# Performance work log

Hardware: AMD Instinct MI355X
Metric: run time of the kernel (lower is better)

## Reference

```python
import jax, jax.numpy as jnp
import numpy as np

N = 1_000_000          # total nodes (atoms)
F = 32                 # node feature dim
K = 16                 # kernels per degree
DEG_COUNTS = [200_000, 300_000, 300_000, 200_000]  # focal nodes per degree 1..4
EPS = 1e-8


def _unit(a):
    # L2-normalize along last axis (CosineSimilarity semantics)
    return a / (jnp.linalg.norm(a, axis=-1, keepdims=True) + EPS)


def setup_inputs() -> dict:
    key = jax.random.key(0)
    ks = jax.random.split(key, 16)
    x = jax.random.normal(ks[0], (N, F), dtype=jnp.float32)
    # selected indices: disjoint partition of all nodes by degree (a permutation)
    perm = jax.random.permutation(ks[1], N)
    sels, off = [], 0
    for c in DEG_COUNTS:
        sels.append(perm[off:off + c].astype(jnp.int64))
        off += c
    inp = {"x": x}
    for d in range(1, 5):
        inp[f"selected_index_deg{d}"] = sels[d - 1]
        inp[f"nei_index_deg{d}"] = jax.random.randint(
            ks[1 + d], (d * DEG_COUNTS[d - 1],), 0, N).astype(jnp.int64)
        inp[f"W_focal{d}"] = jax.random.normal(ks[7 + d], (K, F), dtype=jnp.float32)
        inp[f"W_nei{d}"] = jax.random.normal(ks[11 + d], (K, d, F), dtype=jnp.float32)
    return inp


def _degree_score(x, sel, nei, Wf, Wn, deg):
    # gather receptive field for this degree group
    x_focal = _unit(x[sel])                         # (Nd, F)
    x_nei = _unit(x[nei].reshape(-1, deg, F))       # (Nd, deg, F)
    sc_f = _unit(Wf) @ x_focal.T                    # (K, Nd) cosine vs focal kernel
    sc_n = jnp.einsum('kdf,ndf->kn', _unit(Wn), x_nei) / deg  # mean neighbor cosine
    return sc_f + sc_n                              # (K, Nd)


def reference(x,
              W_focal1, W_nei1, W_focal2, W_nei2,
              W_focal3, W_nei3, W_focal4, W_nei4,
              selected_index_deg1, selected_index_deg2,
              selected_index_deg3, selected_index_deg4,
              nei_index_deg1, nei_index_deg2,
              nei_index_deg3, nei_index_deg4):
    sels = [selected_index_deg1, selected_index_deg2,
            selected_index_deg3, selected_index_deg4]
    neis = [nei_index_deg1, nei_index_deg2, nei_index_deg3, nei_index_deg4]
    Wfs = [W_focal1, W_focal2, W_focal3, W_focal4]
    Wns = [W_nei1, W_nei2, W_nei3, W_nei4]

    out = jnp.zeros((4 * K, N), dtype=x.dtype)  # the `zeros` score matrix
    row, col = 0, 0
    for d in range(1, 5):
        sc = _degree_score(x, sels[d - 1], neis[d - 1], Wfs[d - 1], Wns[d - 1], d)
        nd = sels[d - 1].shape[0]
        out = out.at[row:row + K, col:col + nd].set(sc)
        row += K
        col += nd
    # reorder columns back to original node order (get_reorder_index -> sort)
    order = jnp.argsort(jnp.concatenate(sels))
    return out[:, order].T  # (N, 4*K)
```

## Files before the change

kernel.cpp:

```cpp
#include <hip/hip_runtime.h>
#include <math.h>

#define F 32
#define K 16
#define EPSN 1e-8f
#define NPB 512
#define NPB_FB 256


typedef _Float16 half8 __attribute__((ext_vector_type(8)));
typedef float f32x4  __attribute__((ext_vector_type(4)));
typedef int   i32x2  __attribute__((ext_vector_type(2)));
typedef int   i32x4  __attribute__((ext_vector_type(4)));

#define VMWAIT(N) do { asm volatile("s_waitcnt vmcnt(%0)" :: "n"(N) : "memory"); \
                       __builtin_amdgcn_sched_barrier(0); } while (0)

__global__ __launch_bounds__(256)
void norm_x_kernel(const float* __restrict__ x, _Float16* __restrict__ xh,
                   int nrows)
{
    const int t   = blockIdx.x * 256 + threadIdx.x;
    const int row = t >> 2;
    const int p   = t & 3;
    if (row >= nrows) return;
    const float* xr = x + (size_t)row * F + p * 8;
    const float4 a0 = *(const float4*)xr;
    const float4 a1 = *(const float4*)(xr + 4);
    float ss = a0.x*a0.x + a0.y*a0.y + a0.z*a0.z + a0.w*a0.w
             + a1.x*a1.x + a1.y*a1.y + a1.z*a1.z + a1.w*a1.w;
    ss += __shfl_xor(ss, 1);
    ss += __shfl_xor(ss, 2);
    const float sc = 1.f / (sqrtf(ss) + EPSN);
    half8 h;
    h[0] = (_Float16)(a0.x * sc); h[1] = (_Float16)(a0.y * sc);
    h[2] = (_Float16)(a0.z * sc); h[3] = (_Float16)(a0.w * sc);
    h[4] = (_Float16)(a1.x * sc); h[5] = (_Float16)(a1.y * sc);
    h[6] = (_Float16)(a1.z * sc); h[7] = (_Float16)(a1.w * sc);
    *(half8*)(xh + (size_t)row * F + p * 8) = h;
}

__device__ __forceinline__ void gload16(half8& d, const _Float16* xh,
                                        unsigned row, int kq) {
    const unsigned off = row * 64u + (unsigned)kq * 16u;
    asm volatile("global_load_dwordx4 %0, %1, %2"
                 : "=&v"(d) : "v"(off), "s"(xh) : "memory");
}

__device__ __forceinline__ void gstore(float* out, unsigned off, f32x4 v) {
    asm volatile("global_store_dwordx4 %0, %1, %2"
                 :: "v"(off), "v"(v), "s"(out) : "memory");
}

template<int DEG> struct Idx;
template<> struct Idx<1> { int node; int n0;
    __device__ __forceinline__ int nb(int) const { return n0; } };
template<> struct Idx<2> { int node; i32x2 nn;
    __device__ __forceinline__ int nb(int j) const { return nn[j]; } };
template<> struct Idx<3> { int node; i32x2 nn; int n2;
    __device__ __forceinline__ int nb(int j) const { return j < 2 ? nn[j] : n2; } };
template<> struct Idx<4> { int node; i32x4 nn;
    __device__ __forceinline__ int nb(int j) const { return nn[j]; } };

template<int DEG>
__device__ __forceinline__ void load_idx(Idx<DEG>& d, const int* sel,
                                         const int* nei, int ic) {
    const unsigned so = (unsigned)ic << 2;
    asm volatile("global_load_dword %0, %1, %2"
                 : "=&v"(d.node) : "v"(so), "s"(sel) : "memory");
    const unsigned no = (unsigned)(ic * DEG) << 2;
    if constexpr (DEG == 1)
        asm volatile("global_load_dword %0, %1, %2"
                     : "=&v"(d.n0) : "v"(no), "s"(nei) : "memory");
    else if constexpr (DEG == 2)
        asm volatile("global_load_dwordx2 %0, %1, %2"
                     : "=&v"(d.nn) : "v"(no), "s"(nei) : "memory");
    else if constexpr (DEG == 3) {
        asm volatile("global_load_dwordx2 %0, %1, %2"
                     : "=&v"(d.nn) : "v"(no), "s"(nei) : "memory");
        asm volatile("global_load_dword %0, %1, %2 offset:8"
                     : "=&v"(d.n2) : "v"(no), "s"(nei) : "memory");
    } else
        asm volatile("global_load_dwordx4 %0, %1, %2"
                     : "=&v"(d.nn) : "v"(no), "s"(nei) : "memory");
}

__device__ __forceinline__ f32x4 slab2(half8 b, f32x4 acc,
                                       const _Float16* sWh,
                                       const _Float16* sWl,
                                       int lane, int r) {
    const int aoff = r * 512 + lane * 8;
    const half8 ah = *(const half8*)(sWh + aoff);
    const half8 al = *(const half8*)(sWl + aoff);
    acc = __builtin_amdgcn_mfma_f32_16x16x32_f16(ah, b, acc, 0, 0, 0);
    acc = __builtin_amdgcn_mfma_f32_16x16x32_f16(al, b, acc, 0, 0, 0);
    return acc;
}

template<int DEG>
__device__ __forceinline__ void process_deg(const _Float16* __restrict__ xh,
                                            const int*   __restrict__ sel,
                                            const int*   __restrict__ nei,
                                            const float* __restrict__ Wf,
                                            const float* __restrict__ Wn,
                                            float* __restrict__ out,
                                            int nd, int i0,
                                            _Float16* sWh, _Float16* sWl)
{
    constexpr int R  = DEG + 1;
    constexpr int H  = (DEG <= 2) ? 1 : 2;
    constexpr int C0 = H;
    constexpr int C1 = R - H;
    constexpr int NI = (DEG == 3) ? 3 : 2;
    constexpr int KB = C1 + NI;
    constexpr int KD = C0;
    constexpr int NW = K * R;
    constexpr int ITERS = NPB / 64;
    const int tid = threadIdx.x;

    if (tid < NW) {
        const float* src = (tid < K) ? (Wf + tid * F) : (Wn + (tid - K) * F);
        float ss = 0.f;
        #pragma unroll
        for (int f = 0; f < F; ++f) { const float t = src[f]; ss += t * t; }
        const int t = tid - K;
        const int r = (tid < K) ? 0   : (1 + t % DEG);
        const int k = (tid < K) ? tid : (t / DEG);
        const float sc = (1.f / (sqrtf(ss) + EPSN))
                       * ((r == 0) ? 1.f : 1.f / (float)DEG);
        #pragma unroll
        for (int f = 0; f < F; ++f) {
            const float wv = src[f] * sc;
            const _Float16 hi = (_Float16)wv;
            const _Float16 lo = (_Float16)(wv - (float)hi);
            const int off = r * 512 + (k + 16 * (f >> 3)) * 8 + (f & 7);
            sWh[off] = hi; sWl[off] = lo;
        }
    }
    __syncthreads();

    const int lane = tid & 63;
    const int wv   = tid >> 6;
    const int jcol = lane & 15;
    const int kq   = lane >> 4;
    const int i0w  = i0 + wv * 16 + jcol;

    half8 g0[H], g1[R - H];
    const f32x4 zed = {0.f, 0.f, 0.f, 0.f};

    Idx<DEG> ix, iy;
    { const int ic = (i0w < nd) ? i0w : (nd - 1);
      load_idx<DEG>(ix, sel, nei, ic); }
    { const int i1 = i0w + 64; const int ic = (i1 < nd) ? i1 : (nd - 1);
      load_idx<DEG>(iy, sel, nei, ic); }
    VMWAIT(NI);
    #pragma unroll
    for (int r = 0; r < H; ++r)
        gload16(g0[r], xh, (unsigned)((r == 0) ? ix.node : ix.nb(r-1)), kq);

#define ITER(T, XC, YN)                                                        \
    {                                                                          \
        const int nodeT = XC.node;                                             \
        _Pragma("unroll")                                                      \
        for (int r = H; r < R; ++r)                        \
            gload16(g1[r - H], xh, (unsigned)XC.nb(r-1), kq);                  \
        { const int ii = i0w + ((T) + 2) * 64;         \
          load_idx<DEG>(XC, sel, nei, (ii < nd) ? ii : (nd - 1)); }            \
        VMWAIT(KB);                            \
        f32x4 acc = {0.f, 0.f, 0.f, 0.f};                                      \
        _Pragma("unroll")                                                      \
        for (int r = 0; r < H; ++r)                                            \
            acc = slab2(g0[r], acc, sWh, sWl, lane, r);                        \
        _Pragma("unroll")                                                      \
        for (int r = 0; r < H; ++r)                      \
            gload16(g0[r], xh,                                                 \
                    (unsigned)((r == 0) ? YN.node : YN.nb(r-1)), kq);          \
        VMWAIT(KD);                                      \
        _Pragma("unroll")                                                      \
        for (int r = H; r < R; ++r)                                            \
            acc = slab2(g1[r - H], acc, sWh, sWl, lane, r);                    \
        if (i0w + (T) * 64 < nd) {                           \
            const unsigned ob = (unsigned)nodeT * 256u + (unsigned)kq * 16u;   \
            _Pragma("unroll")                                                  \
            for (int b = 0; b < 4; ++b)                                        \
                gstore(out, ob + (unsigned)b * 64u,                            \
                       (b == DEG - 1) ? acc : zed);                            \
        }                                                                      \
    }

    #pragma unroll 1
    for (int tp = 0; tp < ITERS; tp += 2) {
        ITER(tp,     ix, iy);
        ITER(tp + 1, iy, ix);
    }
#undef ITER
    VMWAIT(0);
}

struct Args {
    const _Float16* xh;
    const int*   sel[4];
    const int*   nei[4];
    const float* Wf[4];
    const float* Wn[4];
    int nd[4];
    int bcum[4];
};

__global__ __launch_bounds__(256, 2)
void fused_kernel(Args a, float* __restrict__ out)
{
    __shared__ __align__(16) _Float16 sWh[5 * 512];
    __shared__ __align__(16) _Float16 sWl[5 * 512];
    const int bid = blockIdx.x;

    if (bid < a.bcum[0]) {
        process_deg<1>(a.xh, a.sel[0], a.nei[0], a.Wf[0], a.Wn[0], out,
                       a.nd[0], bid * NPB, sWh, sWl);
    } else if (bid < a.bcum[1]) {
        process_deg<2>(a.xh, a.sel[1], a.nei[1], a.Wf[1], a.Wn[1], out,
                       a.nd[1], (bid - a.bcum[0]) * NPB, sWh, sWl);
    } else if (bid < a.bcum[2]) {
        process_deg<3>(a.xh, a.sel[2], a.nei[2], a.Wf[2], a.Wn[2], out,
                       a.nd[2], (bid - a.bcum[1]) * NPB, sWh, sWl);
    } else {
        process_deg<4>(a.xh, a.sel[3], a.nei[3], a.Wf[3], a.Wn[3], out,
                       a.nd[3], (bid - a.bcum[2]) * NPB, sWh, sWl);
    }
}

template<int DEG>
__device__ __forceinline__ void process_fb(const float* __restrict__ x,
                                           const int*   __restrict__ sel,
                                           const int*   __restrict__ nei,
                                           const float* __restrict__ Wf,
                                           const float* __restrict__ Wn,
                                           float* __restrict__ out,
                                           int nd, int i0,
                                           _Float16* sWh, _Float16* sWl)
{
    constexpr int R  = 1 + DEG;
    constexpr int NW = K * R;
    const int tid = threadIdx.x;
    if (tid < NW) {
        const float* src = (tid < K) ? (Wf + tid * F) : (Wn + (tid - K) * F);
        float ss = 0.f;
        #pragma unroll
        for (int f = 0; f < F; ++f) { const float t = src[f]; ss += t * t; }
        const float sc = 1.f / (sqrtf(ss) + EPSN);
        const int t = tid - K;
        const int r = (tid < K) ? 0   : (1 + t % DEG);
        const int k = (tid < K) ? tid : (t / DEG);
        #pragma unroll
        for (int f = 0; f < F; ++f) {
            const float wv = src[f] * sc;
            const _Float16 hi = (_Float16)wv;
            const _Float16 lo = (_Float16)(wv - (float)hi);
            const int off = r * 512 + (k + 16 * (f >> 3)) * 8 + (f & 7);
            sWh[off] = hi; sWl[off] = lo;
        }
    }
    __syncthreads();

    const int lane = tid & 63, wv = tid >> 6;
    const int jcol = lane & 15, kq = lane >> 4;
    const float invdeg = 1.f / (float)DEG;

    #pragma unroll 1
    for (int it = 0; it < NPB_FB / 64; ++it) {
        int i = i0 + it * 64 + wv * 16 + jcol;
        const bool valid = (i < nd);
        if (!valid) i = nd - 1;
        const int node = sel[i];
        int nn[DEG];
        #pragma unroll
        for (int j = 0; j < DEG; ++j) nn[j] = nei[i * DEG + j];
        f32x4 acc = {0.f, 0.f, 0.f, 0.f};
        #pragma unroll
        for (int r = 0; r < R; ++r) {
            const unsigned row = (unsigned)((r == 0) ? node : nn[r - 1]);
            const float* xr = x + row * (unsigned)F + kq * 8;
            const float4 a0 = *(const float4*)(xr);
            const float4 a1 = *(const float4*)(xr + 4);
            float ss = a0.x*a0.x + a0.y*a0.y + a0.z*a0.z + a0.w*a0.w
                     + a1.x*a1.x + a1.y*a1.y + a1.z*a1.z + a1.w*a1.w;
            ss += __shfl_xor(ss, 16);
            ss += __shfl_xor(ss, 32);
            float sc = 1.f / (sqrtf(ss) + EPSN);
            if (r > 0) sc *= invdeg;
            const float f0 = a0.x*sc, f1 = a0.y*sc, f2 = a0.z*sc, f3 = a0.w*sc;
            const float f4 = a1.x*sc, f5 = a1.y*sc, f6 = a1.z*sc, f7 = a1.w*sc;
            half8 bh, bl;
            bh[0]=(_Float16)f0; bl[0]=(_Float16)(f0-(float)bh[0]);
            bh[1]=(_Float16)f1; bl[1]=(_Float16)(f1-(float)bh[1]);
            bh[2]=(_Float16)f2; bl[2]=(_Float16)(f2-(float)bh[2]);
            bh[3]=(_Float16)f3; bl[3]=(_Float16)(f3-(float)bh[3]);
            bh[4]=(_Float16)f4; bl[4]=(_Float16)(f4-(float)bh[4]);
            bh[5]=(_Float16)f5; bl[5]=(_Float16)(f5-(float)bh[5]);
            bh[6]=(_Float16)f6; bl[6]=(_Float16)(f6-(float)bh[6]);
            bh[7]=(_Float16)f7; bl[7]=(_Float16)(f7-(float)bh[7]);
            const int aoff = r * 512 + lane * 8;
            const half8 ah = *(const half8*)(sWh + aoff);
            const half8 al = *(const half8*)(sWl + aoff);
            acc = __builtin_amdgcn_mfma_f32_16x16x32_f16(ah, bh, acc, 0, 0, 0);
            acc = __builtin_amdgcn_mfma_f32_16x16x32_f16(ah, bl, acc, 0, 0, 0);
            acc = __builtin_amdgcn_mfma_f32_16x16x32_f16(al, bh, acc, 0, 0, 0);
        }
        if (valid) {
            float* orow = out + (size_t)node * (4 * K);
            #pragma unroll
            for (int b = 0; b < 4; ++b) {
                float4 vst = make_float4(0.f, 0.f, 0.f, 0.f);
                if (b == DEG - 1)
                    vst = make_float4(acc[0], acc[1], acc[2], acc[3]);
                *(float4*)(orow + (b * 4 + kq) * 4) = vst;
            }
        }
    }
}

struct ArgsFb {
    const float* x;
    const int*   sel[4];
    const int*   nei[4];
    const float* Wf[4];
    const float* Wn[4];
    int nd[4];
    int bcum[4];
};

__global__ __launch_bounds__(256)
void fused_kernel_fb(ArgsFb a, float* __restrict__ out)
{
    __shared__ __align__(16) _Float16 sWh[5 * 512];
    __shared__ __align__(16) _Float16 sWl[5 * 512];
    const int bid = blockIdx.x;
    if (bid < a.bcum[0]) {
        process_fb<1>(a.x, a.sel[0], a.nei[0], a.Wf[0], a.Wn[0], out,
                      a.nd[0], bid * NPB_FB, sWh, sWl);
    } else if (bid < a.bcum[1]) {
        process_fb<2>(a.x, a.sel[1], a.nei[1], a.Wf[1], a.Wn[1], out,
                      a.nd[1], (bid - a.bcum[0]) * NPB_FB, sWh, sWl);
    } else if (bid < a.bcum[2]) {
        process_fb<3>(a.x, a.sel[2], a.nei[2], a.Wf[2], a.Wn[2], out,
                      a.nd[2], (bid - a.bcum[1]) * NPB_FB, sWh, sWl);
    } else {
        process_fb<4>(a.x, a.sel[3], a.nei[3], a.Wf[3], a.Wn[3], out,
                      a.nd[3], (bid - a.bcum[2]) * NPB_FB, sWh, sWl);
    }
}

extern "C" void kernel_launch(void* const* d_in, const int* in_sizes, int n_in,
                              void* d_out, int out_size, void* d_ws, size_t ws_size,
                              hipStream_t stream)
{
    const float* xp = (const float*)d_in[0];
    const int nrows = in_sizes[0] / F;
    const size_t need = (size_t)nrows * F * sizeof(_Float16);
    float* out = (float*)d_out;

    if (d_ws != nullptr && ws_size >= need) {
        _Float16* xh = (_Float16*)d_ws;
        const int pre_blocks = (nrows * 4 + 255) / 256;
        norm_x_kernel<<<pre_blocks, 256, 0, stream>>>(xp, xh, nrows);

        Args a;
        a.xh = xh;
        int cum = 0;
        for (int d = 0; d < 4; ++d) {
            a.sel[d] = (const int*)  d_in[1 + 4 * d];
            a.nei[d] = (const int*)  d_in[2 + 4 * d];
            a.Wf[d]  = (const float*)d_in[3 + 4 * d];
            a.Wn[d]  = (const float*)d_in[4 + 4 * d];
            a.nd[d]  = in_sizes[1 + 4 * d];
            cum += (a.nd[d] + NPB - 1) / NPB;
            a.bcum[d] = cum;
        }
        fused_kernel<<<cum, 256, 0, stream>>>(a, out);
    } else {
        ArgsFb a;
        a.x = xp;
        int cum = 0;
        for (int d = 0; d < 4; ++d) {
            a.sel[d] = (const int*)  d_in[1 + 4 * d];
            a.nei[d] = (const int*)  d_in[2 + 4 * d];
            a.Wf[d]  = (const float*)d_in[3 + 4 * d];
            a.Wn[d]  = (const float*)d_in[4 + 4 * d];
            a.nd[d]  = in_sizes[1 + 4 * d];
            cum += (a.nd[d] + NPB_FB - 1) / NPB_FB;
            a.bcum[d] = cum;
        }
        fused_kernel_fb<<<cum, 256, 0, stream>>>(a, out);
    }
}
```

Measured before the change: 463.0 us.

## Hoist weight fragments into registers, double nodes per block, grid-stride normalization

The kernel now loads the hi/lo fp16 weight fragments from LDS into registers once per wave, instead of re-reading them from LDS on every MFMA iteration. Each block processes 1024 nodes instead of 512, so the weight setup and LDS fill are amortized over more work. The normalization pre-pass becomes a grid-stride loop capped at 2048 blocks. Holding the weights in registers raises VGPR pressure, and the larger block size reduces the block count, which may lower occupancy and load balance.

```diff
diff --git a/kernel.cpp b/kernel.cpp
--- a/kernel.cpp
+++ b/kernel.cpp
@@ -4,7 +4,7 @@
 #define F 32
 #define K 16
 #define EPSN 1e-8f
-#define NPB 512
+#define NPB 1024
 #define NPB_FB 256
 
 
@@ -20,24 +20,25 @@
 void norm_x_kernel(const float* __restrict__ x, _Float16* __restrict__ xh,
                    int nrows)
 {
-    const int t   = blockIdx.x * 256 + threadIdx.x;
-    const int row = t >> 2;
-    const int p   = t & 3;
-    if (row >= nrows) return;
-    const float* xr = x + (size_t)row * F + p * 8;
-    const float4 a0 = *(const float4*)xr;
-    const float4 a1 = *(const float4*)(xr + 4);
-    float ss = a0.x*a0.x + a0.y*a0.y + a0.z*a0.z + a0.w*a0.w
-             + a1.x*a1.x + a1.y*a1.y + a1.z*a1.z + a1.w*a1.w;
-    ss += __shfl_xor(ss, 1);
-    ss += __shfl_xor(ss, 2);
-    const float sc = 1.f / (sqrtf(ss) + EPSN);
-    half8 h;
-    h[0] = (_Float16)(a0.x * sc); h[1] = (_Float16)(a0.y * sc);
-    h[2] = (_Float16)(a0.z * sc); h[3] = (_Float16)(a0.w * sc);
-    h[4] = (_Float16)(a1.x * sc); h[5] = (_Float16)(a1.y * sc);
-    h[6] = (_Float16)(a1.z * sc); h[7] = (_Float16)(a1.w * sc);
-    *(half8*)(xh + (size_t)row * F + p * 8) = h;
+    const int stride = gridDim.x * 256;
+    for (int t = blockIdx.x * 256 + threadIdx.x; t < nrows * 4; t += stride) {
+        const int row = t >> 2;
+        const int p   = t & 3;
+        const float* xr = x + (size_t)row * F + p * 8;
+        const float4 a0 = *(const float4*)xr;
+        const float4 a1 = *(const float4*)(xr + 4);
+        float ss = a0.x*a0.x + a0.y*a0.y + a0.z*a0.z + a0.w*a0.w
+                 + a1.x*a1.x + a1.y*a1.y + a1.z*a1.z + a1.w*a1.w;
+        ss += __shfl_xor(ss, 1);
+        ss += __shfl_xor(ss, 2);
+        const float sc = 1.f / (sqrtf(ss) + EPSN);
+        half8 h;
+        h[0] = (_Float16)(a0.x * sc); h[1] = (_Float16)(a0.y * sc);
+        h[2] = (_Float16)(a0.z * sc); h[3] = (_Float16)(a0.w * sc);
+        h[4] = (_Float16)(a1.x * sc); h[5] = (_Float16)(a1.y * sc);
+        h[6] = (_Float16)(a1.z * sc); h[7] = (_Float16)(a1.w * sc);
+        *(half8*)(xh + (size_t)row * F + p * 8) = h;
+    }
 }
 
 __device__ __forceinline__ void gload16(half8& d, const _Float16* xh,
@@ -85,18 +86,6 @@
                      : "=&v"(d.nn) : "v"(no), "s"(nei) : "memory");
 }
 
-__device__ __forceinline__ f32x4 slab2(half8 b, f32x4 acc,
-                                       const _Float16* sWh,
-                                       const _Float16* sWl,
-                                       int lane, int r) {
-    const int aoff = r * 512 + lane * 8;
-    const half8 ah = *(const half8*)(sWh + aoff);
-    const half8 al = *(const half8*)(sWl + aoff);
-    acc = __builtin_amdgcn_mfma_f32_16x16x32_f16(ah, b, acc, 0, 0, 0);
-    acc = __builtin_amdgcn_mfma_f32_16x16x32_f16(al, b, acc, 0, 0, 0);
-    return acc;
-}
-
 template<int DEG>
 __device__ __forceinline__ void process_deg(const _Float16* __restrict__ xh,
                                             const int*   __restrict__ sel,
@@ -144,6 +133,13 @@
     const int jcol = lane & 15;
     const int kq   = lane >> 4;
     const int i0w  = i0 + wv * 16 + jcol;
+
+    half8 wh[R], wl[R];
+    #pragma unroll
+    for (int r = 0; r < R; ++r) {
+        wh[r] = *(const half8*)(sWh + r * 512 + lane * 8);
+        wl[r] = *(const half8*)(sWl + r * 512 + lane * 8);
+    }
 
     half8 g0[H], g1[R - H];
     const f32x4 zed = {0.f, 0.f, 0.f, 0.f};
@@ -169,16 +165,24 @@
         VMWAIT(KB);                            \
         f32x4 acc = {0.f, 0.f, 0.f, 0.f};                                      \
         _Pragma("unroll")                                                      \
-        for (int r = 0; r < H; ++r)                                            \
-            acc = slab2(g0[r], acc, sWh, sWl, lane, r);                        \
+        for (int r = 0; r < H; ++r) {                                          \
+            acc = __builtin_amdgcn_mfma_f32_16x16x32_f16(wh[r], g0[r], acc,    \
+                                                         0, 0, 0);             \
+            acc = __builtin_amdgcn_mfma_f32_16x16x32_f16(wl[r], g0[r], acc,    \
+                                                         0, 0, 0);             \
+        }                                                                      \
         _Pragma("unroll")                                                      \
         for (int r = 0; r < H; ++r)                      \
             gload16(g0[r], xh,                                                 \
                     (unsigned)((r == 0) ? YN.node : YN.nb(r-1)), kq);          \
         VMWAIT(KD);                                      \
         _Pragma("unroll")                                                      \
-        for (int r = H; r < R; ++r)                                            \
-            acc = slab2(g1[r - H], acc, sWh, sWl, lane, r);                    \
+        for (int r = H; r < R; ++r) {                                          \
+            acc = __builtin_amdgcn_mfma_f32_16x16x32_f16(wh[r], g1[r - H],     \
+                                                         acc, 0, 0, 0);        \
+            acc = __builtin_amdgcn_mfma_f32_16x16x32_f16(wl[r], g1[r - H],     \
+                                                         acc, 0, 0, 0);        \
+        }                                                                      \
         if (i0w + (T) * 64 < nd) {                           \
             const unsigned ob = (unsigned)nodeT * 256u + (unsigned)kq * 16u;   \
             _Pragma("unroll")                                                  \
@@ -361,7 +365,8 @@
 
     if (d_ws != nullptr && ws_size >= need) {
         _Float16* xh = (_Float16*)d_ws;
-        const int pre_blocks = (nrows * 4 + 255) / 256;
+        int pre_blocks = (nrows * 4 + 255) / 256;
+        if (pre_blocks > 2048) pre_blocks = 2048;
         norm_x_kernel<<<pre_blocks, 256, 0, stream>>>(xp, xh, nrows);
 
         Args a;
```

Result: no change. 465.7 us (+0.6%).
